# Performance work log

Hardware: AMD Instinct MI355X
Metric: run time of the kernel (lower is better)

Reference implementation:

```python
import jax, jax.numpy as jnp
import numpy as np

EMBED = 1024
HEADS = 16
HEAD_DIM = EMBED // HEADS


def setup_inputs() -> dict:
    key = jax.random.key(0)
    ks = jax.random.split(key, 6)
    B, T, C = 4, 2048, EMBED
    x = jax.random.normal(ks[0], (B, T, C), dtype=jnp.float32)
    # random binary mask [B,1,1,T]; keep at least one valid key per row by forcing first position to 1
    mask = jax.random.randint(ks[1], (B, 1, 1, T), 0, 2, dtype=jnp.int32)
    mask = mask.at[..., 0].set(1)
    scale = 1.0 / np.sqrt(C)
    qkv_w = jax.random.normal(ks[2], (3 * C, C), dtype=jnp.float32) * scale  # torch Linear weight [out,in]
    qkv_b = jax.random.normal(ks[3], (3 * C,), dtype=jnp.float32) * scale
    out_w = jax.random.normal(ks[4], (C, C), dtype=jnp.float32) * scale
    out_b = jax.random.normal(ks[5], (C,), dtype=jnp.float32) * scale
    return {"x": x, "mask": mask, "qkv_w": qkv_w, "qkv_b": qkv_b, "out_w": out_w, "out_b": out_b}


def reference(x, mask, qkv_w, qkv_b, out_w, out_b):
    B, T, C = x.shape
    H, D = HEADS, HEAD_DIM
    qkv = x @ qkv_w.T + qkv_b  # [B,T,3C]
    qkv = qkv.reshape(B, T, 3, H, D).transpose(2, 0, 3, 1, 4)  # [3,B,H,T,D]
    q, k, v = qkv[0], qkv[1], qkv[2]
    scores = jnp.einsum('bhqd,bhkd->bhqk', q, k) / np.sqrt(D)
    scores = jnp.where(mask == 0, -jnp.inf, scores)
    attn = jax.nn.softmax(scores, axis=-1)
    out = jnp.einsum('bhqk,bhkd->bhqd', attn, v)
    out = out.transpose(0, 2, 1, 3).reshape(B, T, C)
    return out @ out_w.T + out_b
```

## Files before the change

kernel.cpp:

```cpp
#include <hip/hip_runtime.h>
#include <hip/hip_bf16.h>

typedef _Float16 f16;
typedef _Float16 f16x4_t __attribute__((ext_vector_type(4)));
typedef _Float16 f16x8 __attribute__((ext_vector_type(8)));
typedef float f32x4 __attribute__((ext_vector_type(4)));

#define AS1(p) ((const __attribute__((address_space(1))) void*)(p))
#define AS3(p) ((__attribute__((address_space(3))) void*)(p))

__device__ __forceinline__ void gload_lds16(const f16* g, f16* l) {
    __builtin_amdgcn_global_load_lds(AS1(g), AS3(l), 16, 0, 0);
}

__device__ __forceinline__ f16x8 cvt8(float4 u, float4 v) {
    f16x8 r;
    r[0] = (f16)u.x; r[1] = (f16)u.y; r[2] = (f16)u.z; r[3] = (f16)u.w;
    r[4] = (f16)v.x; r[5] = (f16)v.y; r[6] = (f16)v.z; r[7] = (f16)v.w;
    return r;
}

#define Q_SCALE 0.180336880111f

__global__ __launch_bounds__(256) void pre_pass(
    const float* __restrict__ x, const float* __restrict__ qw,
    const float* __restrict__ ow, const int* __restrict__ mask,
    f16* __restrict__ x16, f16* __restrict__ w16, f16* __restrict__ ow16,
    int* __restrict__ gpos, int* __restrict__ nkv)
{
    const int blk = blockIdx.x;
    if (blk >= 2048) {
        const int b = blk - 2048;
        if (threadIdx.x < 64) {
            const int lane = threadIdx.x;
            const int* mb = mask + b * 2048;
            int run = 0;
            for (int c = 0; c < 2048; c += 64) {
                int v = (mb[c + lane] != 0) ? 1 : 0;
                unsigned long long bits = __ballot(v);
                int pre = __popcll(bits & ((1ull << lane) - 1ull));
                if (v) gpos[b * 2048 + run + pre] = c + lane;
                run += __popcll(bits);
            }
            if (lane == 0) nkv[b] = run;
        }
        return;
    }
    const int nx8 = 8192 * 1024 / 8;
    const int nw8 = 3072 * 1024 / 8;
    const int no8 = 1024 * 1024 / 8;
    int idx = blk * 256 + threadIdx.x;
    const int stride = 2048 * 256;
    for (int i = idx; i < nx8 + nw8 + no8; i += stride) {
        const float* s; f16* d;
        if (i < nx8)            { size_t o = (size_t)i * 8;                s = x  + o; d = x16  + o; }
        else if (i < nx8 + nw8) { size_t o = (size_t)(i - nx8) * 8;        s = qw + o; d = w16  + o; }
        else                    { size_t o = (size_t)(i - nx8 - nw8) * 8;  s = ow + o; d = ow16 + o; }
        float4 u = *(const float4*)s;
        float4 v = *(const float4*)(s + 4);
        *(f16x8*)d = cvt8(u, v);
    }
}

__global__ __launch_bounds__(256) void gemm_qkv_f16(
    const f16* __restrict__ x16, const f16* __restrict__ w16,
    const float* __restrict__ bias, const int* __restrict__ gpos,
    const int* __restrict__ nkv, f16* __restrict__ q_g,
    f16* __restrict__ k_g, f16* __restrict__ vt_g)
{
    constexpr int BK = 64, K = 1024, NT = K / BK;
    __shared__ f16 As[2][128 * BK], Bs[2][128 * BK];

    const int tid  = threadIdx.x;
    const int lane = tid & 63, wave = tid >> 6;
    const int wy = wave >> 1, wx = wave & 1;
    const int lrow = lane & 15, quad = lane >> 4;
    const int srow = lane >> 3;
    const int sgrp = lane & 7;
    const int x0 = ((quad)     ^ (lrow & 7)) * 8;
    const int x1 = ((4 + quad) ^ (lrow & 7)) * 8;

    const int bx = blockIdx.x, by = blockIdx.y;
    const int z = (bx >= 8);
    int b_kv = 0, mt = 0, nk = 0, nbase, n0;
    if (!z) {
        nbase = 0; n0 = bx * 128;
    } else {
        b_kv = by >> 4; mt = by & 15;
        nk = nkv[b_kv];
        if (mt * 128 >= nk) return;
        nbase = 1024; n0 = (bx - 8) * 128;
    }

    const f16* arow[4];
    const f16* brow[4];
#pragma unroll
    for (int j = 0; j < 4; ++j) {
        int rit = (wave * 4 + j) * 8 + srow;
        int trow;
        if (!z) {
            trow = by * 128 + rit;
        } else {
            int ct = mt * 128 + rit;
            int t = (ct < nk) ? gpos[b_kv * 2048 + ct] : 0;
            trow = b_kv * 2048 + t;
        }
        arow[j] = x16 + (size_t)trow * K + (sgrp ^ srow) * 8;
        brow[j] = w16 + (size_t)(nbase + n0 + rit) * K + (sgrp ^ srow) * 8;
    }

    auto stage = [&](int k0, int bsel) {
#pragma unroll
        for (int j = 0; j < 4; ++j) {
            int rg = wave * 4 + j;
            gload_lds16(arow[j] + k0, &As[bsel][rg * 512 + lane * 8]);
            gload_lds16(brow[j] + k0, &Bs[bsel][rg * 512 + lane * 8]);
        }
    };

    f32x4 acc[4][4] = {};

    stage(0, 0);
    stage(BK, 1);
    asm volatile("s_waitcnt vmcnt(8)" ::: "memory");
    __builtin_amdgcn_s_barrier();

    for (int kt = 0; kt < NT; ++kt) {
        const int cur = kt & 1;

        f16x8 a0[4], a1[4], b0[4], b1[4];
#pragma unroll
        for (int i = 0; i < 4; ++i) {
            const int r = (wy * 64 + i * 16 + lrow) * BK;
            a0[i] = *(const f16x8*)&As[cur][r + x0];
            a1[i] = *(const f16x8*)&As[cur][r + x1];
        }
#pragma unroll
        for (int j = 0; j < 4; ++j) {
            const int r = (wx * 64 + j * 16 + lrow) * BK;
            b0[j] = *(const f16x8*)&Bs[cur][r + x0];
            b1[j] = *(const f16x8*)&Bs[cur][r + x1];
        }
        __builtin_amdgcn_s_setprio(1);
#pragma unroll
        for (int i = 0; i < 4; ++i)
#pragma unroll
            for (int j = 0; j < 4; ++j) {
                acc[i][j] = __builtin_amdgcn_mfma_f32_16x16x32_f16(a0[i], b0[j], acc[i][j], 0, 0, 0);
                acc[i][j] = __builtin_amdgcn_mfma_f32_16x16x32_f16(a1[i], b1[j], acc[i][j], 0, 0, 0);
            }
        __builtin_amdgcn_s_setprio(0);

        __builtin_amdgcn_s_barrier();
        if (kt + 2 < NT) {
            stage((kt + 2) * BK, cur);
            asm volatile("s_waitcnt vmcnt(8)" ::: "memory");
        } else {
            asm volatile("s_waitcnt vmcnt(0)" ::: "memory");
        }
        __builtin_amdgcn_s_barrier();
    }

    if (!z) {
#pragma unroll
        for (int i = 0; i < 4; ++i) {
            size_t row = (size_t)by * 128 + wy * 64 + i * 16 + quad * 4;
            int b = (int)(row >> 11);
            int t = (int)(row & 2047);
#pragma unroll
            for (int j = 0; j < 4; ++j) {
                int col = n0 + wx * 64 + j * 16 + lrow;
                float bb = bias[col];
                int hh = col >> 6, d = col & 63;
                size_t o = ((size_t)(b * 16 + hh) * 2048 + t) * 64 + d;
#pragma unroll
                for (int r = 0; r < 4; ++r)
                    q_g[o + (size_t)r * 64] = (f16)((acc[i][j][r] + bb) * Q_SCALE);
            }
        }
    } else {
        const int region = n0 >> 10;
#pragma unroll
        for (int i = 0; i < 4; ++i) {
            int ct = mt * 128 + wy * 64 + i * 16 + quad * 4;
#pragma unroll
            for (int j = 0; j < 4; ++j) {
                int col = n0 + wx * 64 + j * 16 + lrow;
                float bb = bias[1024 + col];
                int cl = col & 1023, hh = cl >> 6, d = cl & 63;
                size_t bh = (size_t)(b_kv * 16 + hh);
                if (region == 0) {
#pragma unroll
                    for (int r = 0; r < 4; ++r)
                        k_g[(bh * 2048 + ct + r) * 64 + d] = (f16)(acc[i][j][r] + bb);
                } else {
                    f16x4_t pv;
#pragma unroll
                    for (int r = 0; r < 4; ++r) pv[r] = (f16)(acc[i][j][r] + bb);
                    *(f16x4_t*)&vt_g[(bh * 64 + d) * 2048 + ct] = pv;
                }
            }
        }
    }
}

__global__ __launch_bounds__(256) void gemm2_f16(
    const f16* __restrict__ A16, const f16* __restrict__ Bw16,
    const float* __restrict__ bias, float* __restrict__ C,
    int M, int N, int K)
{
    constexpr int BK = 64;
    __shared__ f16 As[2][128 * BK], Bs[2][128 * BK];

    const int tid  = threadIdx.x;
    const int lane = tid & 63, wave = tid >> 6;
    const int wy = wave >> 1, wx = wave & 1;
    const int lrow = lane & 15, quad = lane >> 4;
    const size_t m0 = (size_t)blockIdx.y * 128;
    const size_t n0 = (size_t)blockIdx.x * 128;
    const int srow = lane >> 3, sgrp = lane & 7;
    const int x0 = ((quad)     ^ (lrow & 7)) * 8;
    const int x1 = ((4 + quad) ^ (lrow & 7)) * 8;

    const f16* arow[4];
    const f16* brow[4];
#pragma unroll
    for (int j = 0; j < 4; ++j) {
        int rit = (wave * 4 + j) * 8 + srow;
        arow[j] = A16  + (m0 + rit) * (size_t)K + (sgrp ^ srow) * 8;
        brow[j] = Bw16 + (n0 + rit) * (size_t)K + (sgrp ^ srow) * 8;
    }

    auto stage = [&](int k0, int bsel) {
#pragma unroll
        for (int j = 0; j < 4; ++j) {
            int rg = wave * 4 + j;
            gload_lds16(arow[j] + k0, &As[bsel][rg * 512 + lane * 8]);
            gload_lds16(brow[j] + k0, &Bs[bsel][rg * 512 + lane * 8]);
        }
    };

    f32x4 acc[4][4] = {};
    const int NT = K / BK;

    stage(0, 0);
    stage(BK, 1);
    asm volatile("s_waitcnt vmcnt(8)" ::: "memory");
    __builtin_amdgcn_s_barrier();

    for (int kt = 0; kt < NT; ++kt) {
        const int cur = kt & 1;

        f16x8 a0[4], a1[4], b0[4], b1[4];
#pragma unroll
        for (int i = 0; i < 4; ++i) {
            const int r = (wy * 64 + i * 16 + lrow) * BK;
            a0[i] = *(const f16x8*)&As[cur][r + x0];
            a1[i] = *(const f16x8*)&As[cur][r + x1];
        }
#pragma unroll
        for (int j = 0; j < 4; ++j) {
            const int r = (wx * 64 + j * 16 + lrow) * BK;
            b0[j] = *(const f16x8*)&Bs[cur][r + x0];
            b1[j] = *(const f16x8*)&Bs[cur][r + x1];
        }
        __builtin_amdgcn_s_setprio(1);
#pragma unroll
        for (int i = 0; i < 4; ++i)
#pragma unroll
            for (int j = 0; j < 4; ++j) {
                acc[i][j] = __builtin_amdgcn_mfma_f32_16x16x32_f16(a0[i], b0[j], acc[i][j], 0, 0, 0);
                acc[i][j] = __builtin_amdgcn_mfma_f32_16x16x32_f16(a1[i], b1[j], acc[i][j], 0, 0, 0);
            }
        __builtin_amdgcn_s_setprio(0);

        __builtin_amdgcn_s_barrier();
        if (kt + 2 < NT) {
            stage((kt + 2) * BK, cur);
            asm volatile("s_waitcnt vmcnt(8)" ::: "memory");
        } else {
            asm volatile("s_waitcnt vmcnt(0)" ::: "memory");
        }
        __builtin_amdgcn_s_barrier();
    }

#pragma unroll
    for (int i = 0; i < 4; ++i) {
        size_t row = m0 + wy * 64 + i * 16 + quad * 4;
#pragma unroll
        for (int j = 0; j < 4; ++j) {
            size_t col = n0 + wx * 64 + j * 16 + lrow;
            float bb = bias[col];
#pragma unroll
            for (int r = 0; r < 4; ++r)
                C[(row + r) * N + col] = acc[i][j][r] + bb;
        }
    }
}

__global__ __launch_bounds__(256) void attn_f16(
    const f16* __restrict__ q_g, const f16* __restrict__ k_g,
    const f16* __restrict__ vt_g, const int* __restrict__ nkv,
    f16* __restrict__ att, int B, int T)
{
    constexpr int LDP = 72;
    __shared__ f16 Ks_s[2][64 * 64];
    __shared__ f16 Vt_s[2][64 * 64];
    __shared__ f16 Pt[128 * LDP];

    const int tid  = threadIdx.x;
    const int lane = tid & 63, wave = tid >> 6;
    const int lrow = lane & 15, quad = lane >> 4;
    const int bid = ((int)blockIdx.x & 7) * 128 + ((int)blockIdx.x >> 3);
    const int qt = bid & 15;
    const int h  = (bid >> 4) & 15;
    const int b  = bid >> 8;
    const size_t base = (size_t)b * T;
    const size_t bh = (size_t)(b * 16 + h);
    const f16* qg_base = q_g  + bh * (2048 * 64);
    const f16* kg_base = k_g  + bh * (2048 * 64);
    const f16* vt_base = vt_g + bh * (64 * 2048);

    const int nk = nkv[b];
    const int ntiles = (nk + 63) >> 6;

    const int x0 = ((quad)     ^ (lrow & 7)) * 8;
    const int x1 = ((4 + quad) ^ (lrow & 7)) * 8;

    f16x8 aq[2][2];
#pragma unroll
    for (int qi = 0; qi < 2; ++qi)
#pragma unroll
        for (int ks = 0; ks < 2; ++ks)
            aq[qi][ks] = *(const f16x8*)&qg_base[
                (size_t)(qt * 128 + wave * 32 + qi * 16 + lrow) * 64 + ks * 32 + quad * 8];

    f32x4 oacc[2][4] = {};
    float l_part[2] = {0.f, 0.f};

    const int srow0 = (lane >> 3);
    const int sgrp  = (lane & 7);

    auto stage = [&](int kt, int bsel) {
        const f16* kT = kg_base + kt * 4096;
#pragma unroll
        for (int j = 0; j < 2; ++j) {
            int rg  = wave + j * 4;
            int row = rg * 8 + srow0;
            int grp = sgrp ^ (row & 7);
            gload_lds16(&kT[row * 64 + grp * 8], &Ks_s[bsel][rg * 512 + lane * 8]);
            gload_lds16(&vt_base[(size_t)row * 2048 + kt * 64 + grp * 8],
                        &Vt_s[bsel][rg * 512 + lane * 8]);
        }
    };

    stage(0, 0);
    stage(1, 1);
    asm volatile("s_waitcnt vmcnt(4)" ::: "memory");
    __builtin_amdgcn_s_barrier();

    for (int kt = 0; kt < ntiles; ++kt) {
        const int cur = kt & 1;
        const f16* Ks = Ks_s[cur];
        const f16* Vt = Vt_s[cur];

        f32x4 s[2][4];
        __builtin_amdgcn_s_setprio(1);
#pragma unroll
        for (int ni = 0; ni < 4; ++ni) {
            const int key = ni * 16 + lrow;
            f16x8 k0 = *(const f16x8*)&Ks[key * 64 + x0];
            f16x8 k1 = *(const f16x8*)&Ks[key * 64 + x1];
#pragma unroll
            for (int qi = 0; qi < 2; ++qi) {
                f32x4 t = {0.f, 0.f, 0.f, 0.f};
                t = __builtin_amdgcn_mfma_f32_16x16x32_f16(k0, aq[qi][0], t, 0, 0, 0);
                t = __builtin_amdgcn_mfma_f32_16x16x32_f16(k1, aq[qi][1], t, 0, 0, 0);
                s[qi][ni] = t;
            }
        }
        __builtin_amdgcn_s_setprio(0);

        const int rem = nk - kt * 64;
        auto softmax = [&](bool masked) {
#pragma unroll
            for (int qi = 0; qi < 2; ++qi)
#pragma unroll
                for (int ni = 0; ni < 4; ++ni) {
                    float p[4];
#pragma unroll
                    for (int r = 0; r < 4; ++r) {
                        float e = __builtin_amdgcn_exp2f(s[qi][ni][r]);
                        p[r] = (!masked || (ni * 16 + quad * 4 + r) < rem) ? e : 0.f;
                    }
                    l_part[qi] += (p[0] + p[1]) + (p[2] + p[3]);
                    f16x4_t pk;
#pragma unroll
                    for (int r = 0; r < 4; ++r) pk[r] = (f16)p[r];
                    *(f16x4_t*)&Pt[(wave * 32 + qi * 16 + lrow) * LDP + ni * 16 + quad * 4] = pk;
                }
        };
        if (rem >= 64) softmax(false); else softmax(true);

        f16x8 pf[2][2];
#pragma unroll
        for (int qi = 0; qi < 2; ++qi)
#pragma unroll
            for (int ks = 0; ks < 2; ++ks)
                pf[qi][ks] = *(const f16x8*)&Pt[(wave * 32 + qi * 16 + lrow) * LDP + ks * 32 + quad * 8];
        __builtin_amdgcn_s_setprio(1);
#pragma unroll
        for (int di = 0; di < 4; ++di) {
            const int d = di * 16 + lrow;
            f16x8 v0 = *(const f16x8*)&Vt[d * 64 + x0];
            f16x8 v1 = *(const f16x8*)&Vt[d * 64 + x1];
#pragma unroll
            for (int qi = 0; qi < 2; ++qi) {
                oacc[qi][di] = __builtin_amdgcn_mfma_f32_16x16x32_f16(v0, pf[qi][0], oacc[qi][di], 0, 0, 0);
                oacc[qi][di] = __builtin_amdgcn_mfma_f32_16x16x32_f16(v1, pf[qi][1], oacc[qi][di], 0, 0, 0);
            }
        }
        __builtin_amdgcn_s_setprio(0);

        __builtin_amdgcn_s_barrier();
        if (kt + 2 < ntiles) {
            stage(kt + 2, cur);
            asm volatile("s_waitcnt vmcnt(4)" ::: "memory");
        } else {
            asm volatile("s_waitcnt vmcnt(0)" ::: "memory");
        }
        __builtin_amdgcn_s_barrier();
    }

#pragma unroll
    for (int qi = 0; qi < 2; ++qi) {
        float v = l_part[qi];
        v += __shfl_xor(v, 16);
        v += __shfl_xor(v, 32);
        float inv = 1.f / v;
        int q = qt * 128 + wave * 32 + qi * 16 + lrow;
#pragma unroll
        for (int di = 0; di < 4; ++di) {
            f16x4_t o;
#pragma unroll
            for (int r = 0; r < 4; ++r) o[r] = (f16)(oacc[qi][di][r] * inv);
            *(f16x4_t*)&att[(base + q) * 1024 + h * 64 + di * 16 + quad * 4] = o;
        }
    }
}

extern "C" void kernel_launch(void* const* d_in, const int* in_sizes, int n_in,
                              void* d_out, int out_size, void* d_ws, size_t ws_size,
                              hipStream_t stream) {
    const float* x     = (const float*)d_in[0];
    const int*   mask  = (const int*)d_in[1];
    const float* qkv_w = (const float*)d_in[2];
    const float* qkv_b = (const float*)d_in[3];
    const float* out_w = (const float*)d_in[4];
    const float* out_b = (const float*)d_in[5];
    float* out = (float*)d_out;

    const int B = 4, T = 2048;
    const int M = B * T;
    char* ws = (char*)d_ws;
    f16* q_g = (f16*)(ws);
    f16* k_g = (f16*)(ws + 16777216);
    f16* vt  = (f16*)(ws + 33554432);
    f16* att = (f16*)(ws + 50331648);

    f16* x16  = (f16*)d_out;
    f16* w16  = (f16*)((char*)d_out + 16777216);
    f16* ow16 = (f16*)((char*)d_out + 23068672);
    int* gpos = (int*)((char*)d_out + 25165824);
    int* nkv  = gpos + 4 * 2048;

    dim3 blk(256);
    pre_pass<<<dim3(2052), blk, 0, stream>>>(x, qkv_w, out_w, mask, x16, w16, ow16, gpos, nkv);
    gemm_qkv_f16<<<dim3(24, 64), blk, 0, stream>>>(x16, w16, qkv_b, gpos, nkv, q_g, k_g, vt);
    attn_f16<<<dim3(B * 16 * 16), blk, 0, stream>>>(q_g, k_g, vt, nkv, att, B, T);
    gemm2_f16<<<dim3(1024 / 128, M / 128), blk, 0, stream>>>(att, ow16, out_b, out, M, 1024, 1024);
}
```

Baseline: 251.1 us.

## Enlarge QKV GEMM tiles to 256x256 with 512-thread blocks

The QKV projection GEMM moves from 128x128 tiles on 256 threads to 256x256 tiles on 512 threads (8 waves in a 2x4 grid, each computing 128x64) over a flattened 1D grid of 384 blocks. Each wave now holds 8x4 accumulators and loads A fragments per row inside the MFMA loop. The larger tile is meant to cut global and LDS traffic per FLOP. In exchange it doubles LDS use to 128 KB per block, raises register pressure, and leaves fewer blocks to spread over the CUs. The K/V compaction tiles are also coarser, which may waste more work on rows past the valid-key count.

```diff
diff --git a/kernel.cpp b/kernel.cpp
--- a/kernel.cpp
+++ b/kernel.cpp
@@ -62,34 +62,41 @@
     }
 }
 
-__global__ __launch_bounds__(256) void gemm_qkv_f16(
+__global__ __launch_bounds__(512) void gemm_qkv_f16(
     const f16* __restrict__ x16, const f16* __restrict__ w16,
     const float* __restrict__ bias, const int* __restrict__ gpos,
     const int* __restrict__ nkv, f16* __restrict__ q_g,
     f16* __restrict__ k_g, f16* __restrict__ vt_g)
 {
     constexpr int BK = 64, K = 1024, NT = K / BK;
-    __shared__ f16 As[2][128 * BK], Bs[2][128 * BK];
+    __shared__ f16 As[2][256 * BK], Bs[2][256 * BK];
 
     const int tid  = threadIdx.x;
     const int lane = tid & 63, wave = tid >> 6;
-    const int wy = wave >> 1, wx = wave & 1;
+    const int wr = wave >> 2, wc = wave & 3;
     const int lrow = lane & 15, quad = lane >> 4;
     const int srow = lane >> 3;
     const int sgrp = lane & 7;
     const int x0 = ((quad)     ^ (lrow & 7)) * 8;
     const int x1 = ((4 + quad) ^ (lrow & 7)) * 8;
 
-    const int bx = blockIdx.x, by = blockIdx.y;
-    const int z = (bx >= 8);
+    const int tile = blockIdx.x;
     int b_kv = 0, mt = 0, nk = 0, nbase, n0;
+    size_t m0 = 0;
+    const int z = (tile >= 128);
     if (!z) {
-        nbase = 0; n0 = bx * 128;
+        nbase = 0;
+        m0 = (size_t)(tile >> 2) * 256;
+        n0 = (tile & 3) * 256;
     } else {
-        b_kv = by >> 4; mt = by & 15;
+        int t2 = tile - 128;
+        b_kv = t2 >> 6;
+        int rr = t2 & 63;
+        mt = rr >> 3;
+        n0 = (rr & 7) * 256;
         nk = nkv[b_kv];
-        if (mt * 128 >= nk) return;
-        nbase = 1024; n0 = (bx - 8) * 128;
+        if (mt * 256 >= nk) return;
+        nbase = 1024;
     }
 
     const f16* arow[4];
@@ -99,9 +106,9 @@
         int rit = (wave * 4 + j) * 8 + srow;
         int trow;
         if (!z) {
-            trow = by * 128 + rit;
+            trow = (int)m0 + rit;
         } else {
-            int ct = mt * 128 + rit;
+            int ct = mt * 256 + rit;
             int t = (ct < nk) ? gpos[b_kv * 2048 + ct] : 0;
             trow = b_kv * 2048 + t;
         }
@@ -118,7 +125,7 @@
         }
     };
 
-    f32x4 acc[4][4] = {};
+    f32x4 acc[8][4] = {};
 
     stage(0, 0);
     stage(BK, 1);
@@ -128,27 +135,25 @@
     for (int kt = 0; kt < NT; ++kt) {
         const int cur = kt & 1;
 
-        f16x8 a0[4], a1[4], b0[4], b1[4];
-#pragma unroll
-        for (int i = 0; i < 4; ++i) {
-            const int r = (wy * 64 + i * 16 + lrow) * BK;
-            a0[i] = *(const f16x8*)&As[cur][r + x0];
-            a1[i] = *(const f16x8*)&As[cur][r + x1];
-        }
+        f16x8 b0[4], b1[4];
 #pragma unroll
         for (int j = 0; j < 4; ++j) {
-            const int r = (wx * 64 + j * 16 + lrow) * BK;
+            const int r = (wc * 64 + j * 16 + lrow) * BK;
             b0[j] = *(const f16x8*)&Bs[cur][r + x0];
             b1[j] = *(const f16x8*)&Bs[cur][r + x1];
         }
         __builtin_amdgcn_s_setprio(1);
 #pragma unroll
-        for (int i = 0; i < 4; ++i)
+        for (int i = 0; i < 8; ++i) {
+            const int r = (wr * 128 + i * 16 + lrow) * BK;
+            f16x8 a0 = *(const f16x8*)&As[cur][r + x0];
+            f16x8 a1 = *(const f16x8*)&As[cur][r + x1];
 #pragma unroll
             for (int j = 0; j < 4; ++j) {
-                acc[i][j] = __builtin_amdgcn_mfma_f32_16x16x32_f16(a0[i], b0[j], acc[i][j], 0, 0, 0);
-                acc[i][j] = __builtin_amdgcn_mfma_f32_16x16x32_f16(a1[i], b1[j], acc[i][j], 0, 0, 0);
-            }
+                acc[i][j] = __builtin_amdgcn_mfma_f32_16x16x32_f16(a0, b0[j], acc[i][j], 0, 0, 0);
+                acc[i][j] = __builtin_amdgcn_mfma_f32_16x16x32_f16(a1, b1[j], acc[i][j], 0, 0, 0);
+            }
+        }
         __builtin_amdgcn_s_setprio(0);
 
         __builtin_amdgcn_s_barrier();
@@ -163,13 +168,13 @@
 
     if (!z) {
 #pragma unroll
-        for (int i = 0; i < 4; ++i) {
-            size_t row = (size_t)by * 128 + wy * 64 + i * 16 + quad * 4;
+        for (int i = 0; i < 8; ++i) {
+            size_t row = m0 + wr * 128 + i * 16 + quad * 4;
             int b = (int)(row >> 11);
             int t = (int)(row & 2047);
 #pragma unroll
             for (int j = 0; j < 4; ++j) {
-                int col = n0 + wx * 64 + j * 16 + lrow;
+                int col = n0 + wc * 64 + j * 16 + lrow;
                 float bb = bias[col];
                 int hh = col >> 6, d = col & 63;
                 size_t o = ((size_t)(b * 16 + hh) * 2048 + t) * 64 + d;
@@ -181,11 +186,11 @@
     } else {
         const int region = n0 >> 10;
 #pragma unroll
-        for (int i = 0; i < 4; ++i) {
-            int ct = mt * 128 + wy * 64 + i * 16 + quad * 4;
+        for (int i = 0; i < 8; ++i) {
+            int ct = mt * 256 + wr * 128 + i * 16 + quad * 4;
 #pragma unroll
             for (int j = 0; j < 4; ++j) {
-                int col = n0 + wx * 64 + j * 16 + lrow;
+                int col = n0 + wc * 64 + j * 16 + lrow;
                 float bb = bias[1024 + col];
                 int cl = col & 1023, hh = cl >> 6, d = cl & 63;
                 size_t bh = (size_t)(b_kv * 16 + hh);
@@ -476,7 +481,7 @@
 
     dim3 blk(256);
     pre_pass<<<dim3(2052), blk, 0, stream>>>(x, qkv_w, out_w, mask, x16, w16, ow16, gpos, nkv);
-    gemm_qkv_f16<<<dim3(24, 64), blk, 0, stream>>>(x16, w16, qkv_b, gpos, nkv, q_g, k_g, vt);
+    gemm_qkv_f16<<<dim3(384), dim3(512), 0, stream>>>(x16, w16, qkv_b, gpos, nkv, q_g, k_g, vt);
     attn_f16<<<dim3(B * 16 * 16), blk, 0, stream>>>(q_g, k_g, vt, nkv, att, B, T);
     gemm2_f16<<<dim3(1024 / 128, M / 128), blk, 0, stream>>>(att, ow16, out_b, out, M, 1024, 1024);
 }
```

New measurement: 260.9 us. +3.9%, slower.

## Load GEMM B operand directly from global into registers, skipping LDS staging

Applied to the files above, without the earlier changes.

Both the QKV and output-projection GEMMs stop staging the weight (B) tile through shared memory. Each lane now reads its MFMA B fragments straight from global memory every k-step, and only the A tile stays double-buffered in LDS via global_load_lds. This halves shared-memory use and removes the LDS writes and reads for B, which may allow more resident blocks. In exchange, the B loads are not prefetched, so their global latency sits on the critical path each iteration, and the two wave rows now fetch the same B data twice.

```diff
diff --git a/kernel.cpp b/kernel.cpp
--- a/kernel.cpp
+++ b/kernel.cpp
@@ -69,7 +69,7 @@
     f16* __restrict__ k_g, f16* __restrict__ vt_g)
 {
     constexpr int BK = 64, K = 1024, NT = K / BK;
-    __shared__ f16 As[2][128 * BK], Bs[2][128 * BK];
+    __shared__ f16 As[2][128 * BK];
 
     const int tid  = threadIdx.x;
     const int lane = tid & 63, wave = tid >> 6;
@@ -93,7 +93,7 @@
     }
 
     const f16* arow[4];
-    const f16* brow[4];
+    const f16* bcol[4];
 #pragma unroll
     for (int j = 0; j < 4; ++j) {
         int rit = (wave * 4 + j) * 8 + srow;
@@ -106,41 +106,39 @@
             trow = b_kv * 2048 + t;
         }
         arow[j] = x16 + (size_t)trow * K + (sgrp ^ srow) * 8;
-        brow[j] = w16 + (size_t)(nbase + n0 + rit) * K + (sgrp ^ srow) * 8;
+        bcol[j] = w16 + (size_t)(nbase + n0 + wx * 64 + j * 16 + lrow) * K + quad * 8;
     }
 
     auto stage = [&](int k0, int bsel) {
 #pragma unroll
-        for (int j = 0; j < 4; ++j) {
-            int rg = wave * 4 + j;
-            gload_lds16(arow[j] + k0, &As[bsel][rg * 512 + lane * 8]);
-            gload_lds16(brow[j] + k0, &Bs[bsel][rg * 512 + lane * 8]);
-        }
+        for (int j = 0; j < 4; ++j)
+            gload_lds16(arow[j] + k0, &As[bsel][(wave * 4 + j) * 512 + lane * 8]);
     };
 
     f32x4 acc[4][4] = {};
 
     stage(0, 0);
     stage(BK, 1);
-    asm volatile("s_waitcnt vmcnt(8)" ::: "memory");
+    asm volatile("s_waitcnt vmcnt(4)" ::: "memory");
     __builtin_amdgcn_s_barrier();
 
     for (int kt = 0; kt < NT; ++kt) {
         const int cur = kt & 1;
-
-        f16x8 a0[4], a1[4], b0[4], b1[4];
+        const int k0 = kt * BK;
+
+        f16x8 b0[4], b1[4];
+#pragma unroll
+        for (int j = 0; j < 4; ++j) {
+            b0[j] = *(const f16x8*)(bcol[j] + k0);
+            b1[j] = *(const f16x8*)(bcol[j] + k0 + 32);
+        }
+        f16x8 a0[4], a1[4];
 #pragma unroll
         for (int i = 0; i < 4; ++i) {
             const int r = (wy * 64 + i * 16 + lrow) * BK;
             a0[i] = *(const f16x8*)&As[cur][r + x0];
             a1[i] = *(const f16x8*)&As[cur][r + x1];
         }
-#pragma unroll
-        for (int j = 0; j < 4; ++j) {
-            const int r = (wx * 64 + j * 16 + lrow) * BK;
-            b0[j] = *(const f16x8*)&Bs[cur][r + x0];
-            b1[j] = *(const f16x8*)&Bs[cur][r + x1];
-        }
         __builtin_amdgcn_s_setprio(1);
 #pragma unroll
         for (int i = 0; i < 4; ++i)
@@ -154,7 +152,7 @@
         __builtin_amdgcn_s_barrier();
         if (kt + 2 < NT) {
             stage((kt + 2) * BK, cur);
-            asm volatile("s_waitcnt vmcnt(8)" ::: "memory");
+            asm volatile("s_waitcnt vmcnt(4)" ::: "memory");
         } else {
             asm volatile("s_waitcnt vmcnt(0)" ::: "memory");
         }
@@ -210,7 +208,7 @@
     int M, int N, int K)
 {
     constexpr int BK = 64;
-    __shared__ f16 As[2][128 * BK], Bs[2][128 * BK];
+    __shared__ f16 As[2][128 * BK];
 
     const int tid  = threadIdx.x;
     const int lane = tid & 63, wave = tid >> 6;
@@ -223,21 +221,18 @@
     const int x1 = ((4 + quad) ^ (lrow & 7)) * 8;
 
     const f16* arow[4];
-    const f16* brow[4];
+    const f16* bcol[4];
 #pragma unroll
     for (int j = 0; j < 4; ++j) {
         int rit = (wave * 4 + j) * 8 + srow;
         arow[j] = A16  + (m0 + rit) * (size_t)K + (sgrp ^ srow) * 8;
-        brow[j] = Bw16 + (n0 + rit) * (size_t)K + (sgrp ^ srow) * 8;
+        bcol[j] = Bw16 + (n0 + wx * 64 + j * 16 + lrow) * (size_t)K + quad * 8;
     }
 
     auto stage = [&](int k0, int bsel) {
 #pragma unroll
-        for (int j = 0; j < 4; ++j) {
-            int rg = wave * 4 + j;
-            gload_lds16(arow[j] + k0, &As[bsel][rg * 512 + lane * 8]);
-            gload_lds16(brow[j] + k0, &Bs[bsel][rg * 512 + lane * 8]);
-        }
+        for (int j = 0; j < 4; ++j)
+            gload_lds16(arow[j] + k0, &As[bsel][(wave * 4 + j) * 512 + lane * 8]);
     };
 
     f32x4 acc[4][4] = {};
@@ -245,25 +240,26 @@
 
     stage(0, 0);
     stage(BK, 1);
-    asm volatile("s_waitcnt vmcnt(8)" ::: "memory");
+    asm volatile("s_waitcnt vmcnt(4)" ::: "memory");
     __builtin_amdgcn_s_barrier();
 
     for (int kt = 0; kt < NT; ++kt) {
         const int cur = kt & 1;
-
-        f16x8 a0[4], a1[4], b0[4], b1[4];
+        const int k0 = kt * BK;
+
+        f16x8 b0[4], b1[4];
+#pragma unroll
+        for (int j = 0; j < 4; ++j) {
+            b0[j] = *(const f16x8*)(bcol[j] + k0);
+            b1[j] = *(const f16x8*)(bcol[j] + k0 + 32);
+        }
+        f16x8 a0[4], a1[4];
 #pragma unroll
         for (int i = 0; i < 4; ++i) {
             const int r = (wy * 64 + i * 16 + lrow) * BK;
             a0[i] = *(const f16x8*)&As[cur][r + x0];
             a1[i] = *(const f16x8*)&As[cur][r + x1];
         }
-#pragma unroll
-        for (int j = 0; j < 4; ++j) {
-            const int r = (wx * 64 + j * 16 + lrow) * BK;
-            b0[j] = *(const f16x8*)&Bs[cur][r + x0];
-            b1[j] = *(const f16x8*)&Bs[cur][r + x1];
-        }
         __builtin_amdgcn_s_setprio(1);
 #pragma unroll
         for (int i = 0; i < 4; ++i)
@@ -277,7 +273,7 @@
         __builtin_amdgcn_s_barrier();
         if (kt + 2 < NT) {
             stage((kt + 2) * BK, cur);
-            asm volatile("s_waitcnt vmcnt(8)" ::: "memory");
+            asm volatile("s_waitcnt vmcnt(4)" ::: "memory");
         } else {
             asm volatile("s_waitcnt vmcnt(0)" ::: "memory");
         }
```

Measured after the change: 309.8 us. 23.4% more time.
